# Kernel optimization log

Hardware: AMD Instinct MI355X
Metric: run time of the kernel (lower is better)

The kernel has to match this reference:

```python
import jax, jax.numpy as jnp
import numpy as np
from jax import lax

H = 666
W = 666
EPS = 1e-5


def _conv(x, w, b):
    # NCHW conv, SAME padding, stride 1
    y = lax.conv_general_dilated(x, w, (1, 1), 'SAME',
                                 dimension_numbers=('NCHW', 'OIHW', 'NCHW'))
    return y + b[None, :, None, None]


def _bn2d(x, g, b):
    m = jnp.mean(x, (0, 2, 3), keepdims=True)
    v = jnp.var(x, (0, 2, 3), keepdims=True)
    return (x - m) * lax.rsqrt(v + EPS) * g[None, :, None, None] + b[None, :, None, None]


def _pool(x):
    return lax.reduce_window(x, -jnp.inf, lax.max, (1, 1, 2, 2), (1, 1, 2, 2), 'VALID')


def setup_inputs() -> dict:
    key = jax.random.key(0)
    ks = jax.random.split(key, 16)
    P, N, D = 20000, 32, 9

    def rn(k, shape, scale=0.05):
        return (jax.random.normal(k, shape, jnp.float32) * scale).astype(jnp.float32)

    return {
        'pillars': jax.random.normal(ks[0], (P, N, D), jnp.float32),
        'coords': jax.random.randint(ks[1], (P, 3), 0, 666, jnp.int64 if jax.config.jax_enable_x64 else jnp.int32),
        # PillarFeatureNet
        'lin_w': rn(ks[2], (64, 9)), 'lin_b': jnp.zeros((64,), jnp.float32),
        'pfn_g': jnp.ones((64,), jnp.float32), 'pfn_b': jnp.zeros((64,), jnp.float32),
        # Backbone
        'c1_w': rn(ks[3], (64, 64, 3, 3)), 'c1_b': jnp.zeros((64,), jnp.float32),
        'bn1_g': jnp.ones((64,), jnp.float32), 'bn1_b': jnp.zeros((64,), jnp.float32),
        'c2_w': rn(ks[4], (128, 64, 3, 3)), 'c2_b': jnp.zeros((128,), jnp.float32),
        'bn2_g': jnp.ones((128,), jnp.float32), 'bn2_b': jnp.zeros((128,), jnp.float32),
        # SSD head
        'h1_w': rn(ks[5], (256, 128, 3, 3)), 'h1_b': jnp.zeros((256,), jnp.float32),
        'hbn_g': jnp.ones((256,), jnp.float32), 'hbn_b': jnp.zeros((256,), jnp.float32),
        'hb_w': rn(ks[6], (21, 256, 3, 3)), 'hb_b': jnp.zeros((21,), jnp.float32),
        'hc_w': rn(ks[7], (3, 256, 3, 3)), 'hc_b': jnp.zeros((3,), jnp.float32),
    }


def reference(pillars, coords, lin_w, lin_b, pfn_g, pfn_b,
              c1_w, c1_b, bn1_g, bn1_b, c2_w, c2_b, bn2_g, bn2_b,
              h1_w, h1_b, hbn_g, hbn_b, hb_w, hb_b, hc_w, hc_b):
    P, N, D = pillars.shape
    # --- PillarFeatureNet: Linear -> BN1d (batch stats) -> ReLU -> max over points ---
    x = pillars.reshape(P * N, D) @ lin_w.T + lin_b           # [P*N, 64]
    m = jnp.mean(x, 0)
    v = jnp.var(x, 0)
    x = jax.nn.relu((x - m) * lax.rsqrt(v + EPS) * pfn_g + pfn_b)
    feats = jnp.max(x.reshape(P, N, -1), axis=1)              # [P, 64]

    # --- PseudoImageScatter: one vectorized scatter replacing the per-pillar loop ---
    y_idx = coords[:, 1]
    x_idx = coords[:, 2]
    valid = (y_idx >= 0) & (y_idx < H) & (x_idx >= 0) & (x_idx < W)
    y_idx = jnp.where(valid, y_idx, H)   # OOB -> dropped by scatter
    x_idx = jnp.where(valid, x_idx, W)
    img = jnp.zeros((64, H, W), feats.dtype).at[:, y_idx, x_idx].set(feats.T, mode='drop')
    img = img[None]                                           # [1, 64, H, W]

    # --- Backbone ---
    b1 = _pool(jax.nn.relu(_bn2d(_conv(img, c1_w, c1_b), bn1_g, bn1_b)))   # [1,64,333,333]
    b2 = _pool(jax.nn.relu(_bn2d(_conv(b1, c2_w, c2_b), bn2_g, bn2_b)))    # [1,128,166,166]

    # --- SSD head ---
    h = jax.nn.relu(_bn2d(_conv(b2, h1_w, h1_b), hbn_g, hbn_b))            # [1,256,166,166]
    bbox = _conv(h, hb_w, hb_b)                                            # [1,21,166,166]
    cls = _conv(h, hc_w, hc_b)                                             # [1,3,166,166]
    return (bbox, cls)
```

## Files before the change

kernel.cpp:

```cpp
#include <hip/hip_runtime.h>
#include <hip/hip_bf16.h>
#include <cstdint>
#include <cstddef>

#define BN_EPS 1e-5f

typedef short short8 __attribute__((ext_vector_type(8)));
typedef float float16 __attribute__((ext_vector_type(16)));
typedef unsigned short ushort_t;

__device__ __forceinline__ float bf2f(ushort_t u) {
  return __uint_as_float(((unsigned int)u) << 16);
}
__device__ __forceinline__ ushort_t f2bf(float f) {
  unsigned int u = __float_as_uint(f);
  u += 0x7FFFu + ((u >> 16) & 1u);
  return (ushort_t)(u >> 16);
}


__global__ __launch_bounds__(512) void pillar_moments(
    const float* __restrict__ pillars, float* __restrict__ mom) {
  float S[9], M[45];
#pragma unroll
  for (int i = 0; i < 9; ++i) S[i] = 0.f;
#pragma unroll
  for (int i = 0; i < 45; ++i) M[i] = 0.f;
  const int t = blockIdx.x * 512 + threadIdx.x;
  const int NTH = 128 * 512;
  for (long r = t; r < 640000; r += NTH) {
    float x[9];
    const float* rp = pillars + r * 9;
#pragma unroll
    for (int d = 0; d < 9; ++d) x[d] = rp[d];
    int k = 0;
#pragma unroll
    for (int i = 0; i < 9; ++i) {
      S[i] += x[i];
#pragma unroll
      for (int j = i; j < 9; ++j) { M[k] += x[i] * x[j]; ++k; }
    }
  }
#pragma unroll
  for (int i = 0; i < 9; ++i)
#pragma unroll
    for (int o = 32; o > 0; o >>= 1) S[i] += __shfl_xor(S[i], o);
#pragma unroll
  for (int i = 0; i < 45; ++i)
#pragma unroll
    for (int o = 32; o > 0; o >>= 1) M[i] += __shfl_xor(M[i], o);
  __shared__ float red[8 * 54];
  int lane = threadIdx.x & 63, wv = threadIdx.x >> 6;
  if (lane == 0) {
#pragma unroll
    for (int i = 0; i < 9; ++i) red[wv * 54 + i] = S[i];
#pragma unroll
    for (int i = 0; i < 45; ++i) red[wv * 54 + 9 + i] = M[i];
  }
  __syncthreads();
  if (threadIdx.x < 54) {
    float s = 0.f;
#pragma unroll
    for (int w8 = 0; w8 < 8; ++w8) s += red[w8 * 54 + threadIdx.x];
    atomicAdd(&mom[threadIdx.x], s);
  }
}

__global__ void pfn_finalize(const float* __restrict__ mom,
                             const float* __restrict__ lin_w,
                             const float* __restrict__ lin_b,
                             const float* __restrict__ g, const float* __restrict__ b,
                             float* __restrict__ ss) {
  int c = threadIdx.x;
  double w[9], S[9];
#pragma unroll
  for (int d = 0; d < 9; ++d) {
    w[d] = (double)lin_w[c * 9 + d];
    S[d] = (double)mom[d];
  }
  double wS = 0.0;
#pragma unroll
  for (int d = 0; d < 9; ++d) wS += w[d] * S[d];
  double wMw = 0.0;
  int k = 0;
#pragma unroll
  for (int i = 0; i < 9; ++i)
#pragma unroll
    for (int j = i; j < 9; ++j) {
      double m = (double)mom[9 + k];
      wMw += (i == j ? 1.0 : 2.0) * w[i] * w[j] * m;
      ++k;
    }
  const double N = 640000.0;
  double bc = (double)lin_b[c];
  double mean = (wS + N * bc) / N;
  double ey2 = (wMw + 2.0 * bc * wS + N * bc * bc) / N;
  double var = ey2 - mean * mean;
  if (var < 0.0) var = 0.0;
  double inv = 1.0 / sqrt(var + (double)BN_EPS);
  double sc = (double)g[c] * inv;
  ss[c] = (float)sc;
  ss[c + 64] = (float)((double)b[c] - mean * sc);
}

__global__ __launch_bounds__(256) void pfn_feats(
    const float* __restrict__ pillars, const float* __restrict__ lin_w,
    const float* __restrict__ lin_b, const float* __restrict__ ss,
    ushort_t* __restrict__ feats) {
  __shared__ float s_p[1152];
  int tid = threadIdx.x;
  int c = tid & 63, pe = tid >> 6;
  long pb = (long)blockIdx.x * 4;
  for (int i = tid; i < 1152; i += 256) s_p[i] = pillars[pb * 288 + i];
  float w[9];
#pragma unroll
  for (int d = 0; d < 9; ++d) w[d] = lin_w[c * 9 + d];
  float bl = lin_b[c];
  float sc = ss[c], sh = ss[c + 64];
  __syncthreads();
  const float* pp = &s_p[pe * 288];
  float m = -1e30f;
#pragma unroll 4
  for (int n = 0; n < 32; ++n) {
    float y = bl;
#pragma unroll
    for (int d = 0; d < 9; ++d) y += pp[n * 9 + d] * w[d];
    float v = fmaxf(y * sc + sh, 0.f);
    m = fmaxf(m, v);
  }
  feats[(pb + pe) * 64 + c] = f2bf(m);
}


__global__ void scatter_winner(const int* __restrict__ coords, int* __restrict__ winner,
                               int P) {
  int p = blockIdx.x * 256 + threadIdx.x;
  if (p >= P) return;
  int y = coords[p * 3 + 1], x = coords[p * 3 + 2];
  if (y >= 0 && y < 666 && x >= 0 && x < 666) atomicMax(&winner[y * 666 + x], p);
}


__device__ __forceinline__ void prep_one(const float* __restrict__ w,
                                         ushort_t* __restrict__ w2, int C, int N,
                                         int Ntg, int chunks, int u) {
  int total = chunks * 9 * 2 * Ntg * 64;
  if (u >= total) return;
  int l = u & 63;
  int g = u >> 6;
  int ntg = g % Ntg;
  int g2 = g / Ntg;
  int s = g2 & 1;
  int g3 = g2 >> 1;
  int pos = g3 % 9;
  int cc = g3 / 9;
  int n = ntg * 32 + (l & 31);
  int c0 = cc * 32 + s * 16 + (l >> 5) * 8;
  ushort_t o8[8];
#pragma unroll
  for (int j = 0; j < 8; ++j) {
    int c = c0 + j;
    float v = (n < N && c < C) ? w[((size_t)n * C + c) * 9 + pos] : 0.f;
    o8[j] = f2bf(v);
  }
  *(uint4*)&w2[(size_t)u * 8] = *(const uint4*)o8;
}

__device__ __forceinline__ void prep_head_one(const float* __restrict__ hb,
                                              const float* __restrict__ hc,
                                              ushort_t* __restrict__ w2, int u) {
  int total = 8 * 9 * 2 * 64;
  if (u >= total) return;
  int l = u & 63;
  int g = u >> 6;
  int s = g & 1;
  int g3 = g >> 1;
  int pos = g3 % 9;
  int cc = g3 / 9;
  int n = l & 31;
  int c0 = cc * 32 + s * 16 + (l >> 5) * 8;
  ushort_t o8[8];
#pragma unroll
  for (int j = 0; j < 8; ++j) {
    int c = c0 + j;
    float v = 0.f;
    if (n < 21) v = hb[((size_t)n * 256 + c) * 9 + pos];
    else if (n < 24) v = hc[((size_t)(n - 21) * 256 + c) * 9 + pos];
    o8[j] = f2bf(v);
  }
  *(uint4*)&w2[(size_t)u * 8] = *(const uint4*)o8;
}

__global__ void prep_all(const float* __restrict__ c1_w, const float* __restrict__ c2_w,
                         const float* __restrict__ h1_w, const float* __restrict__ hb_w,
                         const float* __restrict__ hc_w, ushort_t* __restrict__ w2c1,
                         ushort_t* __restrict__ w2c2, ushort_t* __restrict__ w2h1,
                         ushort_t* __restrict__ w2hd) {
  int b = blockIdx.x;
  int t = threadIdx.x;
  if (b < 18) prep_one(c1_w, w2c1, 64, 64, 2, 2, b * 256 + t);
  else if (b < 54) prep_one(c2_w, w2c2, 64, 128, 4, 2, (b - 18) * 256 + t);
  else if (b < 198) prep_one(h1_w, w2h1, 128, 256, 8, 4, (b - 54) * 256 + t);
  else prep_head_one(hb_w, hc_w, w2hd, (b - 198) * 256 + t);
}


__global__ void bn_make_coefs(const float* __restrict__ acc, const float* __restrict__ g,
                              const float* __restrict__ b, float invN,
                              float* __restrict__ coef, int C) {
  int c = threadIdx.x;
  if (c >= C) return;
  float m = acc[c] * invN;
  float v = fmaxf(acc[c + 256] * invN - m * m, 0.f);
  float sc = g[c] * rsqrtf(v + BN_EPS);
  coef[c] = sc;
  coef[C + c] = b[c] - m * sc;
}


template <int NT, int WAVES, int MODE, bool HEAD, bool STATS, bool POOL>
__global__ __launch_bounds__(WAVES * 64, WAVES == 8 ? 4 : 3) void conv_mfma(
    const ushort_t* __restrict__ in, const int* __restrict__ winner,
    const ushort_t* __restrict__ feats, const ushort_t* __restrict__ w2,
    const float* __restrict__ bias, const float* __restrict__ bias2,
    const float* __restrict__ coef_in, ushort_t* __restrict__ obf,
    float* __restrict__ hpart, float* __restrict__ statacc, int W, int H, int C,
    int nchunks, int Ntg) {
  constexpr int NTHREADS = WAVES * 64;
  __shared__ ushort_t s_in[(WAVES + 2) * 66 * 32];
  __shared__ ushort_t s_w[9 * 2 * NT * 512];
  const int tid = threadIdx.x;
  const int lane = tid & 63, wv = tid >> 6;
  const int lc = lane & 31, lh = lane >> 5;
  const int x0 = blockIdx.x * 64, y0 = blockIdx.y * WAVES;
  const int z = blockIdx.z;
  const int cc0 = HEAD ? z * nchunks : 0;
  const int z_oc = HEAD ? 0 : z;

  int pc[2][2][3];
#pragma unroll
  for (int s = 0; s < 2; ++s)
#pragma unroll
    for (int Mt = 0; Mt < 2; ++Mt)
#pragma unroll
      for (int kx = 0; kx < 3; ++kx) {
        int col = Mt * 32 + kx + lc;
        int q = (2 * s + lh) ^ ((col >> 1) & 3);
        pc[s][Mt][kx] = col * 32 + q * 8;
      }

  const int sg = tid & 3;
  const int tpos = tid >> 2;
  constexpr int TPOS = NTHREADS / 4;
  constexpr int NPOS = (WAVES + 2) * 66;
  constexpr int NIT = (NPOS + TPOS - 1) / TPOS;
  int ldst[NIT], gsrc[NIT];
#pragma unroll
  for (int it = 0; it < NIT; ++it) {
    ldst[it] = -1;
    gsrc[it] = -1;
    int p = tpos + it * TPOS;
    if (p < NPOS) {
      int r = p / 66, col = p - r * 66;
      int f = sg ^ ((col >> 1) & 3);
      ldst[it] = (r * 66 + col) * 32 + f * 8;
      int gy = y0 - 1 + r, gx = x0 - 1 + col;
      if (gy >= 0 && gy < H && gx >= 0 && gx < W) {
        if (MODE == 2) {
          int pw = winner[gy * 666 + gx];
          if (pw >= 0) gsrc[it] = pw * 64 + sg * 8;
        } else {
          gsrc[it] = (gy * W + gx) * C + sg * 8;
        }
      }
    }
  }

  float bv[NT];
#pragma unroll
  for (int nt = 0; nt < NT; ++nt) {
    if (HEAD) {
      bv[nt] = (z == 0) ? (lc < 21 ? bias[lc] : (lc < 24 ? bias2[lc - 21] : 0.f)) : 0.f;
    } else {
      bv[nt] = bias[(z * NT + nt) * 32 + lc];
    }
  }
  float16 acc[2][NT];
#pragma unroll
  for (int Mt = 0; Mt < 2; ++Mt)
#pragma unroll
    for (int nt = 0; nt < NT; ++nt)
#pragma unroll
      for (int r = 0; r < 16; ++r) acc[Mt][nt][r] = bv[nt];

  for (int cc = 0; cc < nchunks; ++cc) {
    const int ccg = cc0 + cc;
    __syncthreads();
    if (MODE == 2) {
#pragma unroll
      for (int it = 0; it < NIT; ++it) {
        if (ldst[it] < 0) continue;
        uint4 v = make_uint4(0, 0, 0, 0);
        if (gsrc[it] >= 0) v = *(const uint4*)&feats[gsrc[it] + ccg * 32];
        *(uint4*)&s_in[ldst[it]] = v;
      }
    } else {
      float sc8[8], sh8[8];
      {
        int ch = ccg * 32 + sg * 8;
        float4 a0 = *(const float4*)&coef_in[ch];
        float4 a1 = *(const float4*)&coef_in[ch + 4];
        float4 b0 = *(const float4*)&coef_in[C + ch];
        float4 b1 = *(const float4*)&coef_in[C + ch + 4];
        sc8[0] = a0.x; sc8[1] = a0.y; sc8[2] = a0.z; sc8[3] = a0.w;
        sc8[4] = a1.x; sc8[5] = a1.y; sc8[6] = a1.z; sc8[7] = a1.w;
        sh8[0] = b0.x; sh8[1] = b0.y; sh8[2] = b0.z; sh8[3] = b0.w;
        sh8[4] = b1.x; sh8[5] = b1.y; sh8[6] = b1.z; sh8[7] = b1.w;
      }
#pragma unroll
      for (int it = 0; it < NIT; ++it) {
        if (ldst[it] < 0) continue;
        ushort_t v8[8] = {0, 0, 0, 0, 0, 0, 0, 0};
        if (gsrc[it] >= 0) {
          uint4 raw = *(const uint4*)&in[gsrc[it] + ccg * 32];
          const ushort_t* rp = (const ushort_t*)&raw;
#pragma unroll
          for (int j = 0; j < 8; ++j)
            v8[j] = f2bf(fmaxf(bf2f(rp[j]) * sc8[j] + sh8[j], 0.f));
        }
        *(uint4*)&s_in[ldst[it]] = *(const uint4*)v8;
      }
    }
    const int NW = NT * 1152;
    for (int u = tid; u < NW; u += NTHREADS) {
      int l16 = u & 63, grp = u >> 6;
      int nt = grp % NT, ps = grp / NT;
      const ushort_t* src =
          w2 + ((size_t)((ccg * 18 + ps) * Ntg + z_oc * NT + nt) * 64 + l16) * 8;
      *(uint4*)&s_w[(size_t)u * 8] = *(const uint4*)src;
    }
    __syncthreads();
#pragma unroll
    for (int ky = 0; ky < 3; ++ky) {
      int rowoff = (wv + ky) * (66 * 32);
#pragma unroll
      for (int kx = 0; kx < 3; ++kx) {
        const int pos = ky * 3 + kx;
#pragma unroll
        for (int s = 0; s < 2; ++s) {
          short8 Bf[NT];
#pragma unroll
          for (int nt = 0; nt < NT; ++nt)
            Bf[nt] = *(const short8*)&s_w[((pos * 2 + s) * NT + nt) * 512 + lane * 8];
#pragma unroll
          for (int Mt = 0; Mt < 2; ++Mt) {
            short8 Af = *(const short8*)&s_in[rowoff + pc[s][Mt][kx]];
#pragma unroll
            for (int nt = 0; nt < NT; ++nt)
              acc[Mt][nt] =
                  __builtin_amdgcn_mfma_f32_32x32x16_bf16(Af, Bf[nt], acc[Mt][nt], 0, 0, 0);
          }
        }
      }
    }
  }

  const int y = y0 + wv;
  const bool yok = (y < H);
  const int Ntot = Ntg * 32;

  if (HEAD) {
    if (yok) {
      float* hp = hpart + (size_t)z * (size_t)(H * W) * 32;
#pragma unroll
      for (int Mt = 0; Mt < 2; ++Mt)
#pragma unroll
        for (int r = 0; r < 16; ++r) {
          int m = (r & 3) + 8 * (r >> 2) + 4 * lh;
          int x = x0 + Mt * 32 + m;
          if (x < W) {
            size_t sp = (size_t)y * W + x;
            hp[sp * 32 + lc] = acc[Mt][0][r];
          }
        }
    }
    return;
  }

  if (!POOL) {
    if (yok) {
#pragma unroll
      for (int Mt = 0; Mt < 2; ++Mt)
#pragma unroll
        for (int r = 0; r < 16; ++r) {
          int m = (r & 3) + 8 * (r >> 2) + 4 * lh;
          int x = x0 + Mt * 32 + m;
          if (x < W) {
            size_t sp = (size_t)y * W + x;
#pragma unroll
            for (int nt = 0; nt < NT; ++nt) {
              int oc = (z * NT + nt) * 32 + lc;
              obf[sp * Ntot + oc] = f2bf(acc[Mt][nt][r]);
            }
          }
        }
    }
  }

  if (STATS) {
    float s1[NT], s2[NT];
#pragma unroll
    for (int nt = 0; nt < NT; ++nt) { s1[nt] = 0.f; s2[nt] = 0.f; }
    if (yok) {
#pragma unroll
      for (int Mt = 0; Mt < 2; ++Mt)
#pragma unroll
        for (int r = 0; r < 16; ++r) {
          int m = (r & 3) + 8 * (r >> 2) + 4 * lh;
          int x = x0 + Mt * 32 + m;
          if (x < W) {
#pragma unroll
            for (int nt = 0; nt < NT; ++nt) {
              float v = acc[Mt][nt][r];
              s1[nt] += v;
              s2[nt] += v * v;
            }
          }
        }
    }
#pragma unroll
    for (int nt = 0; nt < NT; ++nt) {
      s1[nt] += __shfl_xor(s1[nt], 32);
      s2[nt] += __shfl_xor(s2[nt], 32);
    }
    __syncthreads();
    float* red = (float*)s_in;
    if (lh == 0) {
#pragma unroll
      for (int nt = 0; nt < NT; ++nt) {
        red[(wv * NT + nt) * 32 + lc] = s1[nt];
        red[WAVES * NT * 32 + (wv * NT + nt) * 32 + lc] = s2[nt];
      }
    }
    __syncthreads();
    if (wv == 0 && lh == 0) {
#pragma unroll
      for (int nt = 0; nt < NT; ++nt) {
        float a = 0.f, b = 0.f;
#pragma unroll
        for (int w8 = 0; w8 < WAVES; ++w8) {
          a += red[(w8 * NT + nt) * 32 + lc];
          b += red[WAVES * NT * 32 + (w8 * NT + nt) * 32 + lc];
        }
        int ch = (z * NT + nt) * 32 + lc;
        atomicAdd(&statacc[ch], a);
        atomicAdd(&statacc[ch + 256], b);
      }
    }
  }

  if (POOL) {
    const int OWp = W >> 1, OHp = H >> 1;
    float hm[2][NT][8];
#pragma unroll
    for (int Mt = 0; Mt < 2; ++Mt)
#pragma unroll
      for (int nt = 0; nt < NT; ++nt)
#pragma unroll
        for (int i = 0; i < 8; ++i)
          hm[Mt][nt][i] = fmaxf(acc[Mt][nt][2 * i], acc[Mt][nt][2 * i + 1]);
    __syncthreads();
    float* pl = (float*)s_in;
    if (wv & 1) {
#pragma unroll
      for (int Mt = 0; Mt < 2; ++Mt)
#pragma unroll
        for (int nt = 0; nt < NT; ++nt)
#pragma unroll
          for (int i = 0; i < 8; ++i)
            pl[((((wv >> 1) * 2 + Mt) * NT + nt) * 8 + i) * 64 + lane] = hm[Mt][nt][i];
    }
    __syncthreads();
    if (!(wv & 1)) {
      int oy = (y0 + wv) >> 1;
      if (oy < OHp) {
#pragma unroll
        for (int Mt = 0; Mt < 2; ++Mt)
#pragma unroll
          for (int i = 0; i < 8; ++i) {
            int pxl = Mt * 16 + (i >> 1) * 4 + (i & 1) + 2 * lh;
            int ox = (x0 >> 1) + pxl;
            if (ox < OWp) {
#pragma unroll
              for (int nt = 0; nt < NT; ++nt) {
                float v = fmaxf(
                    hm[Mt][nt][i],
                    pl[((((wv >> 1) * 2 + Mt) * NT + nt) * 8 + i) * 64 + lane]);
                int oc = (z * NT + nt) * 32 + lc;
                obf[((size_t)oy * OWp + ox) * Ntot + oc] = f2bf(v);
              }
            }
          }
      }
    }
  }
}


__global__ __launch_bounds__(256) void head_reduce(const float* __restrict__ hp,
                                                   float* __restrict__ out, int HW,
                                                   int nz) {
  __shared__ float t[256 * 33];
  int tid = threadIdx.x;
  int sp0 = blockIdx.x * 256;
  int lim = (HW - sp0) * 32;
#pragma unroll 4
  for (int i = 0; i < 32; ++i) {
    int e = i * 256 + tid;
    float s = 0.f;
    if (e < lim) {
      size_t gidx = (size_t)sp0 * 32 + e;
      for (int z = 0; z < nz; ++z) s += hp[(size_t)z * HW * 32 + gidx];
    }
    t[(e >> 5) * 33 + (e & 31)] = s;
  }
  __syncthreads();
  int sp = sp0 + tid;
  if (sp < HW) {
#pragma unroll
    for (int ch = 0; ch < 24; ++ch)
      out[(size_t)ch * HW + sp] = t[tid * 33 + ch];
  }
}


extern "C" void kernel_launch(void* const* d_in, const int* in_sizes, int n_in,
                              void* d_out, int out_size, void* d_ws, size_t ws_size,
                              hipStream_t stream) {
  (void)in_sizes; (void)n_in; (void)out_size; (void)ws_size;
  const float* pillars = (const float*)d_in[0];
  const int* coords = (const int*)d_in[1];
  const float* lin_w = (const float*)d_in[2];
  const float* lin_b = (const float*)d_in[3];
  const float* pfn_g = (const float*)d_in[4];
  const float* pfn_b = (const float*)d_in[5];
  const float* c1_w = (const float*)d_in[6];
  const float* c1_b = (const float*)d_in[7];
  const float* bn1_g = (const float*)d_in[8];
  const float* bn1_b = (const float*)d_in[9];
  const float* c2_w = (const float*)d_in[10];
  const float* c2_b = (const float*)d_in[11];
  const float* bn2_g = (const float*)d_in[12];
  const float* bn2_b = (const float*)d_in[13];
  const float* h1_w = (const float*)d_in[14];
  const float* h1_b = (const float*)d_in[15];
  const float* hbn_g = (const float*)d_in[16];
  const float* hbn_b = (const float*)d_in[17];
  const float* hb_w = (const float*)d_in[18];
  const float* hb_b = (const float*)d_in[19];
  const float* hc_w = (const float*)d_in[20];
  const float* hc_b = (const float*)d_in[21];
  float* out = (float*)d_out;

  char* ws = (char*)d_ws;
  float* mom     = (float*)(ws + 0);
  float* pfn_ss  = (float*)(ws + 512);
  float* bn_acc1 = (float*)(ws + 1024);
  float* bn_acc2 = (float*)(ws + 3072);
  float* bn_acc3 = (float*)(ws + 5120);
  float* coef1   = (float*)(ws + 7168);
  float* coef2   = (float*)(ws + 7680);
  float* coef3   = (float*)(ws + 8704);
  int* winner    = (int*)(ws + 10752);
  ushort_t* feats  = (ushort_t*)(ws + 1785088);
  ushort_t* c1p    = (ushort_t*)(ws + 4345088);
  ushort_t* c2p    = (ushort_t*)(ws + 18538880);
  ushort_t* h1out  = (ushort_t*)(ws + 25593216);
  ushort_t* w2c1   = (ushort_t*)(ws + 39701888);
  ushort_t* w2c2   = (ushort_t*)(ws + 39775616);
  ushort_t* w2h1   = (ushort_t*)(ws + 39923072);
  ushort_t* w2hd   = (ushort_t*)(ws + 40512896);
  float* hpart     = (float*)(ws + 40660352);

  const int HW3 = 166 * 166;

  hipMemsetAsync(ws, 0, 10752, stream);
  hipMemsetAsync(winner, 0xFF, 1774224, stream);

  prep_all<<<234, 256, 0, stream>>>(c1_w, c2_w, h1_w, hb_w, hc_w, w2c1, w2c2, w2h1,
                                    w2hd);

  pillar_moments<<<128, 512, 0, stream>>>(pillars, mom);
  pfn_finalize<<<1, 64, 0, stream>>>(mom, lin_w, lin_b, pfn_g, pfn_b, pfn_ss);
  pfn_feats<<<5000, 256, 0, stream>>>(pillars, lin_w, lin_b, pfn_ss, feats);

  scatter_winner<<<(20000 + 255) / 256, 256, 0, stream>>>(coords, winner, 20000);

  conv_mfma<2, 8, 2, false, true, true><<<dim3(11, 84, 1), 512, 0, stream>>>(
      nullptr, winner, feats, w2c1, c1_b, nullptr, nullptr, c1p, nullptr, bn_acc1, 666,
      666, 64, 2, 2);
  bn_make_coefs<<<1, 64, 0, stream>>>(bn_acc1, bn1_g, bn1_b, 1.f / 443556.f, coef1, 64);

  conv_mfma<2, 8, 1, false, true, true><<<dim3(6, 42, 2), 512, 0, stream>>>(
      c1p, nullptr, nullptr, w2c2, c2_b, nullptr, coef1, c2p, nullptr, bn_acc2, 333, 333,
      64, 2, 4);
  bn_make_coefs<<<1, 128, 0, stream>>>(bn_acc2, bn2_g, bn2_b, 1.f / 110889.f, coef2, 128);

  conv_mfma<2, 4, 1, false, true, false><<<dim3(3, 42, 4), 256, 0, stream>>>(
      c2p, nullptr, nullptr, w2h1, h1_b, nullptr, coef2, h1out, nullptr, bn_acc3, 166,
      166, 128, 4, 8);
  bn_make_coefs<<<1, 256, 0, stream>>>(bn_acc3, hbn_g, hbn_b, 1.f / 27556.f, coef3, 256);

  conv_mfma<1, 4, 1, true, false, false><<<dim3(3, 42, 4), 256, 0, stream>>>(
      h1out, nullptr, nullptr, w2hd, hb_b, hc_b, coef3, nullptr, hpart, nullptr, 166,
      166, 256, 2, 1);
  head_reduce<<<(HW3 + 255) / 256, 256, 0, stream>>>(hpart, out, HW3, 4);
}
```

Before: 322.3 us.

## Split channel chunks into half-staging to shrink LDS and raise conv occupancy

```diff
diff --git a/kernel.cpp b/kernel.cpp
--- a/kernel.cpp
+++ b/kernel.cpp
@@ -218,8 +218,8 @@
 }
 
 
-template <int NT, int WAVES, int MODE, bool HEAD, bool STATS, bool POOL>
-__global__ __launch_bounds__(WAVES * 64, WAVES == 8 ? 4 : 3) void conv_mfma(
+template <int NT, int WAVES, int MODE, bool HEAD, bool STATS, bool POOL, bool SPLIT>
+__global__ __launch_bounds__(WAVES * 64, SPLIT ? 4 : (WAVES == 8 ? 4 : 3)) void conv_mfma(
     const ushort_t* __restrict__ in, const int* __restrict__ winner,
     const ushort_t* __restrict__ feats, const ushort_t* __restrict__ w2,
     const float* __restrict__ bias, const float* __restrict__ bias2,
@@ -227,8 +227,13 @@
     float* __restrict__ hpart, float* __restrict__ statacc, int W, int H, int C,
     int nchunks, int Ntg) {
   constexpr int NTHREADS = WAVES * 64;
-  __shared__ ushort_t s_in[(WAVES + 2) * 66 * 32];
-  __shared__ ushort_t s_w[9 * 2 * NT * 512];
+  constexpr int CPP = SPLIT ? 16 : 32;
+  constexpr int SGN = SPLIT ? 2 : 4;
+  constexpr int SIN = (WAVES + 2) * 66 * CPP;
+  constexpr int SWC = (SPLIT ? 9 : 18) * NT * 512;
+  __shared__ ushort_t s_all[SIN + SWC];
+  ushort_t* s_in = s_all;
+  ushort_t* s_w = s_all + SIN;
   const int tid = threadIdx.x;
   const int lane = tid & 63, wv = tid >> 6;
   const int lc = lane & 31, lh = lane >> 5;
@@ -245,13 +250,18 @@
 #pragma unroll
       for (int kx = 0; kx < 3; ++kx) {
         int col = Mt * 32 + kx + lc;
-        int q = (2 * s + lh) ^ ((col >> 1) & 3);
-        pc[s][Mt][kx] = col * 32 + q * 8;
-      }
-
-  const int sg = tid & 3;
-  const int tpos = tid >> 2;
-  constexpr int TPOS = NTHREADS / 4;
+        if (SPLIT) {
+          int q = lh ^ (col & 1);
+          pc[s][Mt][kx] = col * 16 + q * 8;
+        } else {
+          int q = (2 * s + lh) ^ ((col >> 1) & 3);
+          pc[s][Mt][kx] = col * 32 + q * 8;
+        }
+      }
+
+  const int sg = tid & (SGN - 1);
+  const int tpos = tid / SGN;
+  constexpr int TPOS = NTHREADS / SGN;
   constexpr int NPOS = (WAVES + 2) * 66;
   constexpr int NIT = (NPOS + TPOS - 1) / TPOS;
   int ldst[NIT], gsrc[NIT];
@@ -262,8 +272,8 @@
     int p = tpos + it * TPOS;
     if (p < NPOS) {
       int r = p / 66, col = p - r * 66;
-      int f = sg ^ ((col >> 1) & 3);
-      ldst[it] = (r * 66 + col) * 32 + f * 8;
+      int f = SPLIT ? (sg ^ (col & 1)) : (sg ^ ((col >> 1) & 3));
+      ldst[it] = (r * 66 + col) * CPP + f * 8;
       int gy = y0 - 1 + r, gx = x0 - 1 + col;
       if (gy >= 0 && gy < H && gx >= 0 && gx < W) {
         if (MODE == 2) {
@@ -293,21 +303,20 @@
 #pragma unroll
       for (int r = 0; r < 16; ++r) acc[Mt][nt][r] = bv[nt];
 
-  for (int cc = 0; cc < nchunks; ++cc) {
-    const int ccg = cc0 + cc;
-    __syncthreads();
+  auto stage_in = [&](int ccg, int sh) {
+    const int off = ccg * 32 + (SPLIT ? sh * 16 : 0);
     if (MODE == 2) {
 #pragma unroll
       for (int it = 0; it < NIT; ++it) {
         if (ldst[it] < 0) continue;
         uint4 v = make_uint4(0, 0, 0, 0);
-        if (gsrc[it] >= 0) v = *(const uint4*)&feats[gsrc[it] + ccg * 32];
+        if (gsrc[it] >= 0) v = *(const uint4*)&feats[gsrc[it] + off];
         *(uint4*)&s_in[ldst[it]] = v;
       }
     } else {
       float sc8[8], sh8[8];
       {
-        int ch = ccg * 32 + sg * 8;
+        int ch = off + sg * 8;
         float4 a0 = *(const float4*)&coef_in[ch];
         float4 a1 = *(const float4*)&coef_in[ch + 4];
         float4 b0 = *(const float4*)&coef_in[C + ch];
@@ -322,7 +331,7 @@
         if (ldst[it] < 0) continue;
         ushort_t v8[8] = {0, 0, 0, 0, 0, 0, 0, 0};
         if (gsrc[it] >= 0) {
-          uint4 raw = *(const uint4*)&in[gsrc[it] + ccg * 32];
+          uint4 raw = *(const uint4*)&in[gsrc[it] + off];
           const ushort_t* rp = (const ushort_t*)&raw;
 #pragma unroll
           for (int j = 0; j < 8; ++j)
@@ -331,18 +340,57 @@
         *(uint4*)&s_in[ldst[it]] = *(const uint4*)v8;
       }
     }
-    const int NW = NT * 1152;
-    for (int u = tid; u < NW; u += NTHREADS) {
-      int l16 = u & 63, grp = u >> 6;
-      int nt = grp % NT, ps = grp / NT;
-      const ushort_t* src =
-          w2 + ((size_t)((ccg * 18 + ps) * Ntg + z_oc * NT + nt) * 64 + l16) * 8;
-      *(uint4*)&s_w[(size_t)u * 8] = *(const uint4*)src;
-    }
-    __syncthreads();
+  };
+
+  auto stage_w = [&](int ccg, int sh) {
+    if (SPLIT) {
+      const int NWU = 9 * NT * 64;
+      for (int u = tid; u < NWU; u += NTHREADS) {
+        int l16 = u & 63, grp = u >> 6;
+        int nt = grp % NT, pos = grp / NT;
+        const ushort_t* src =
+            w2 + ((size_t)((ccg * 18 + pos * 2 + sh) * Ntg + z_oc * NT + nt) * 64 + l16) * 8;
+        *(uint4*)&s_w[(size_t)((pos * NT + nt) * 512 + l16 * 8)] = *(const uint4*)src;
+      }
+    } else {
+      const int NW = NT * 1152;
+      for (int u = tid; u < NW; u += NTHREADS) {
+        int l16 = u & 63, grp = u >> 6;
+        int nt = grp % NT, ps = grp / NT;
+        const ushort_t* src =
+            w2 + ((size_t)((ccg * 18 + ps) * Ntg + z_oc * NT + nt) * 64 + l16) * 8;
+        *(uint4*)&s_w[(size_t)u * 8] = *(const uint4*)src;
+      }
+    }
+  };
+
+  auto compute_half = [&]() {
 #pragma unroll
     for (int ky = 0; ky < 3; ++ky) {
-      int rowoff = (wv + ky) * (66 * 32);
+      int rowoff = (wv + ky) * (66 * CPP);
+#pragma unroll
+      for (int kx = 0; kx < 3; ++kx) {
+        const int pos = ky * 3 + kx;
+        short8 Bf[NT];
+#pragma unroll
+        for (int nt = 0; nt < NT; ++nt)
+          Bf[nt] = *(const short8*)&s_w[(pos * NT + nt) * 512 + lane * 8];
+#pragma unroll
+        for (int Mt = 0; Mt < 2; ++Mt) {
+          short8 Af = *(const short8*)&s_in[rowoff + pc[0][Mt][kx]];
+#pragma unroll
+          for (int nt = 0; nt < NT; ++nt)
+            acc[Mt][nt] =
+                __builtin_amdgcn_mfma_f32_32x32x16_bf16(Af, Bf[nt], acc[Mt][nt], 0, 0, 0);
+        }
+      }
+    }
+  };
+
+  auto compute_full = [&]() {
+#pragma unroll
+    for (int ky = 0; ky < 3; ++ky) {
+      int rowoff = (wv + ky) * (66 * CPP);
 #pragma unroll
       for (int kx = 0; kx < 3; ++kx) {
         const int pos = ky * 3 + kx;
@@ -362,6 +410,32 @@
           }
         }
       }
+    }
+  };
+
+  if (SPLIT) {
+    for (int cc = 0; cc < nchunks; ++cc) {
+#pragma unroll
+      for (int sh = 0; sh < 2; ++sh) {
+        __syncthreads();
+        stage_in(cc0 + cc, sh);
+        stage_w(cc0 + cc, sh);
+        __syncthreads();
+        __builtin_amdgcn_s_setprio(1);
+        compute_half();
+        __builtin_amdgcn_s_setprio(0);
+      }
+    }
+  } else {
+    for (int cc = 0; cc < nchunks; ++cc) {
+      const int ccg = cc0 + cc;
+      __syncthreads();
+      stage_in(ccg, 0);
+      stage_w(ccg, 0);
+      __syncthreads();
+      __builtin_amdgcn_s_setprio(1);
+      compute_full();
+      __builtin_amdgcn_s_setprio(0);
     }
   }
 
@@ -434,7 +508,7 @@
       s2[nt] += __shfl_xor(s2[nt], 32);
     }
     __syncthreads();
-    float* red = (float*)s_in;
+    float* red = (float*)s_all;
     if (lh == 0) {
 #pragma unroll
       for (int nt = 0; nt < NT; ++nt) {
@@ -470,7 +544,7 @@
         for (int i = 0; i < 8; ++i)
           hm[Mt][nt][i] = fmaxf(acc[Mt][nt][2 * i], acc[Mt][nt][2 * i + 1]);
     __syncthreads();
-    float* pl = (float*)s_in;
+    float* pl = (float*)s_all;
     if (wv & 1) {
 #pragma unroll
       for (int Mt = 0; Mt < 2; ++Mt)
@@ -596,22 +670,22 @@
 
   scatter_winner<<<(20000 + 255) / 256, 256, 0, stream>>>(coords, winner, 20000);
 
-  conv_mfma<2, 8, 2, false, true, true><<<dim3(11, 84, 1), 512, 0, stream>>>(
+  conv_mfma<2, 4, 2, false, true, true, true><<<dim3(11, 167, 1), 256, 0, stream>>>(
       nullptr, winner, feats, w2c1, c1_b, nullptr, nullptr, c1p, nullptr, bn_acc1, 666,
       666, 64, 2, 2);
   bn_make_coefs<<<1, 64, 0, stream>>>(bn_acc1, bn1_g, bn1_b, 1.f / 443556.f, coef1, 64);
 
-  conv_mfma<2, 8, 1, false, true, true><<<dim3(6, 42, 2), 512, 0, stream>>>(
+  conv_mfma<2, 4, 1, false, true, true, true><<<dim3(6, 84, 2), 256, 0, stream>>>(
       c1p, nullptr, nullptr, w2c2, c2_b, nullptr, coef1, c2p, nullptr, bn_acc2, 333, 333,
       64, 2, 4);
   bn_make_coefs<<<1, 128, 0, stream>>>(bn_acc2, bn2_g, bn2_b, 1.f / 110889.f, coef2, 128);
 
-  conv_mfma<2, 4, 1, false, true, false><<<dim3(3, 42, 4), 256, 0, stream>>>(
+  conv_mfma<2, 4, 1, false, true, false, false><<<dim3(3, 42, 4), 256, 0, stream>>>(
       c2p, nullptr, nullptr, w2h1, h1_b, nullptr, coef2, h1out, nullptr, bn_acc3, 166,
       166, 128, 4, 8);
   bn_make_coefs<<<1, 256, 0, stream>>>(bn_acc3, hbn_g, hbn_b, 1.f / 27556.f, coef3, 256);
 
-  conv_mfma<1, 4, 1, true, false, false><<<dim3(3, 42, 4), 256, 0, stream>>>(
+  conv_mfma<1, 4, 1, true, false, false, false><<<dim3(3, 42, 4), 256, 0, stream>>>(
       h1out, nullptr, nullptr, w2hd, hb_b, hc_b, coef3, nullptr, hpart, nullptr, 166,
       166, 256, 2, 1);
   head_reduce<<<(HW3 + 255) / 256, 256, 0, stream>>>(hpart, out, HW3, 4);
```

After: 350.6 us. 1.09x slower.

## Double-buffer conv staging with direct global-to-LDS loads and separate BN-ReLU pass

Applied to the files above, without the earlier changes.

```diff
diff --git a/kernel.cpp b/kernel.cpp
--- a/kernel.cpp
+++ b/kernel.cpp
@@ -16,6 +16,12 @@
   unsigned int u = __float_as_uint(f);
   u += 0x7FFFu + ((u >> 16) & 1u);
   return (ushort_t)(u >> 16);
+}
+
+__device__ __forceinline__ void gload16(const ushort_t* g, ushort_t* l) {
+  __builtin_amdgcn_global_load_lds(
+      (const __attribute__((address_space(1))) unsigned int*)g,
+      (__attribute__((address_space(3))) unsigned int*)l, 16, 0, 0);
 }
 
 
@@ -218,17 +224,45 @@
 }
 
 
-template <int NT, int WAVES, int MODE, bool HEAD, bool STATS, bool POOL>
-__global__ __launch_bounds__(WAVES * 64, WAVES == 8 ? 4 : 3) void conv_mfma(
+__global__ __launch_bounds__(256) void bnrelu(const ushort_t* __restrict__ inp,
+                                              const float* __restrict__ coef, int C,
+                                              int L8, ushort_t* __restrict__ outp) {
+  __shared__ float sc[512];
+  int tid = threadIdx.x;
+  for (int i = tid; i < 2 * C; i += 256) sc[i] = coef[i];
+  __syncthreads();
+  int t = blockIdx.x * 256 + tid;
+  if (t >= L8) return;
+  size_t e0 = (size_t)t * 8;
+  int c0 = (t << 3) & (C - 1);
+  short8 v = *(const short8*)&inp[e0];
+  const ushort_t* vp = (const ushort_t*)&v;
+  ushort_t o[8];
+#pragma unroll
+  for (int j = 0; j < 8; ++j) {
+    float x = bf2f(vp[j]);
+    o[j] = f2bf(fmaxf(x * sc[c0 + j] + sc[C + c0 + j], 0.f));
+  }
+  *(uint4*)&outp[e0] = *(const uint4*)o;
+}
+
+
+template <int NT, int WAVES, bool GATHER, bool HEAD, bool STATS, bool POOL>
+__global__ __launch_bounds__(WAVES * 64, 4) void conv_mfma(
     const ushort_t* __restrict__ in, const int* __restrict__ winner,
     const ushort_t* __restrict__ feats, const ushort_t* __restrict__ w2,
     const float* __restrict__ bias, const float* __restrict__ bias2,
-    const float* __restrict__ coef_in, ushort_t* __restrict__ obf,
+    const ushort_t* __restrict__ zbuf, ushort_t* __restrict__ obf,
     float* __restrict__ hpart, float* __restrict__ statacc, int W, int H, int C,
     int nchunks, int Ntg) {
   constexpr int NTHREADS = WAVES * 64;
-  __shared__ ushort_t s_in[(WAVES + 2) * 66 * 32];
-  __shared__ ushort_t s_w[9 * 2 * NT * 512];
+  constexpr int NPOS = (WAVES + 2) * 66;
+  constexpr int IN_U4 = NPOS * 2;
+  constexpr int W_U4 = 9 * NT * 64;
+  constexpr int INIT = (IN_U4 + NTHREADS - 1) / NTHREADS;
+  constexpr int WIT = (W_U4 + NTHREADS - 1) / NTHREADS;
+  __shared__ ushort_t s_in[2][IN_U4 * 8];
+  __shared__ ushort_t s_w[2][W_U4 * 8];
   const int tid = threadIdx.x;
   const int lane = tid & 63, wv = tid >> 6;
   const int lc = lane & 31, lh = lane >> 5;
@@ -237,42 +271,44 @@
   const int cc0 = HEAD ? z * nchunks : 0;
   const int z_oc = HEAD ? 0 : z;
 
-  int pc[2][2][3];
-#pragma unroll
-  for (int s = 0; s < 2; ++s)
-#pragma unroll
-    for (int Mt = 0; Mt < 2; ++Mt)
-#pragma unroll
-      for (int kx = 0; kx < 3; ++kx) {
-        int col = Mt * 32 + kx + lc;
-        int q = (2 * s + lh) ^ ((col >> 1) & 3);
-        pc[s][Mt][kx] = col * 32 + q * 8;
-      }
-
-  const int sg = tid & 3;
-  const int tpos = tid >> 2;
-  constexpr int TPOS = NTHREADS / 4;
-  constexpr int NPOS = (WAVES + 2) * 66;
-  constexpr int NIT = (NPOS + TPOS - 1) / TPOS;
-  int ldst[NIT], gsrc[NIT];
-#pragma unroll
-  for (int it = 0; it < NIT; ++it) {
-    ldst[it] = -1;
-    gsrc[it] = -1;
-    int p = tpos + it * TPOS;
-    if (p < NPOS) {
+  int pc[2][3];
+#pragma unroll
+  for (int Mt = 0; Mt < 2; ++Mt)
+#pragma unroll
+    for (int kx = 0; kx < 3; ++kx) {
+      int col = Mt * 32 + kx + lc;
+      pc[Mt][kx] = col * 16 + (lh ^ (col & 1)) * 8;
+    }
+
+  const ushort_t* isrc[INIT];
+#pragma unroll
+  for (int it = 0; it < INIT; ++it) {
+    isrc[it] = zbuf;
+    int d = it * NTHREADS + tid;
+    if (d < IN_U4) {
+      int p = d >> 1, g = d & 1;
       int r = p / 66, col = p - r * 66;
-      int f = sg ^ ((col >> 1) & 3);
-      ldst[it] = (r * 66 + col) * 32 + f * 8;
+      int cg = g ^ (col & 1);
       int gy = y0 - 1 + r, gx = x0 - 1 + col;
       if (gy >= 0 && gy < H && gx >= 0 && gx < W) {
-        if (MODE == 2) {
+        if (GATHER) {
           int pw = winner[gy * 666 + gx];
-          if (pw >= 0) gsrc[it] = pw * 64 + sg * 8;
+          if (pw >= 0) isrc[it] = feats + pw * 64 + cg * 8;
         } else {
-          gsrc[it] = (gy * W + gx) * C + sg * 8;
+          isrc[it] = in + (size_t)(gy * W + gx) * C + cg * 8;
         }
       }
+    }
+  }
+  int wof[WIT];
+#pragma unroll
+  for (int it = 0; it < WIT; ++it) {
+    wof[it] = 0;
+    int d = it * NTHREADS + tid;
+    if (d < W_U4) {
+      int grp = d >> 6, l16 = d & 63;
+      int pos = grp / NT, nt = grp % NT;
+      wof[it] = (pos * 2 * Ntg + z_oc * NT + nt) * 512 + l16 * 8;
     }
   }
 
@@ -293,76 +329,55 @@
 #pragma unroll
       for (int r = 0; r < 16; ++r) acc[Mt][nt][r] = bv[nt];
 
-  for (int cc = 0; cc < nchunks; ++cc) {
-    const int ccg = cc0 + cc;
-    __syncthreads();
-    if (MODE == 2) {
-#pragma unroll
-      for (int it = 0; it < NIT; ++it) {
-        if (ldst[it] < 0) continue;
-        uint4 v = make_uint4(0, 0, 0, 0);
-        if (gsrc[it] >= 0) v = *(const uint4*)&feats[gsrc[it] + ccg * 32];
-        *(uint4*)&s_in[ldst[it]] = v;
-      }
-    } else {
-      float sc8[8], sh8[8];
-      {
-        int ch = ccg * 32 + sg * 8;
-        float4 a0 = *(const float4*)&coef_in[ch];
-        float4 a1 = *(const float4*)&coef_in[ch + 4];
-        float4 b0 = *(const float4*)&coef_in[C + ch];
-        float4 b1 = *(const float4*)&coef_in[C + ch + 4];
-        sc8[0] = a0.x; sc8[1] = a0.y; sc8[2] = a0.z; sc8[3] = a0.w;
-        sc8[4] = a1.x; sc8[5] = a1.y; sc8[6] = a1.z; sc8[7] = a1.w;
-        sh8[0] = b0.x; sh8[1] = b0.y; sh8[2] = b0.z; sh8[3] = b0.w;
-        sh8[4] = b1.x; sh8[5] = b1.y; sh8[6] = b1.z; sh8[7] = b1.w;
-      }
-#pragma unroll
-      for (int it = 0; it < NIT; ++it) {
-        if (ldst[it] < 0) continue;
-        ushort_t v8[8] = {0, 0, 0, 0, 0, 0, 0, 0};
-        if (gsrc[it] >= 0) {
-          uint4 raw = *(const uint4*)&in[gsrc[it] + ccg * 32];
-          const ushort_t* rp = (const ushort_t*)&raw;
-#pragma unroll
-          for (int j = 0; j < 8; ++j)
-            v8[j] = f2bf(fmaxf(bf2f(rp[j]) * sc8[j] + sh8[j], 0.f));
-        }
-        *(uint4*)&s_in[ldst[it]] = *(const uint4*)v8;
-      }
-    }
-    const int NW = NT * 1152;
-    for (int u = tid; u < NW; u += NTHREADS) {
-      int l16 = u & 63, grp = u >> 6;
-      int nt = grp % NT, ps = grp / NT;
-      const ushort_t* src =
-          w2 + ((size_t)((ccg * 18 + ps) * Ntg + z_oc * NT + nt) * 64 + l16) * 8;
-      *(uint4*)&s_w[(size_t)u * 8] = *(const uint4*)src;
-    }
-    __syncthreads();
+  auto stage = [&](int ph, int b) {
+    int ccg = cc0 + (ph >> 1), sh = ph & 1;
+    int coff = ccg * 32 + sh * 16;
+#pragma unroll
+    for (int it = 0; it < INIT; ++it) {
+      int d = it * NTHREADS + tid;
+      if (d < IN_U4)
+        gload16(isrc[it] + coff, &s_in[b][(size_t)(it * NTHREADS + wv * 64) * 8]);
+    }
+    int wbase = (ccg * 18 + sh) * Ntg * 512;
+#pragma unroll
+    for (int it = 0; it < WIT; ++it) {
+      int d = it * NTHREADS + tid;
+      if (d < W_U4)
+        gload16(w2 + wbase + wof[it], &s_w[b][(size_t)(it * NTHREADS + wv * 64) * 8]);
+    }
+  };
+
+  auto compute_phase = [&](int b) {
 #pragma unroll
     for (int ky = 0; ky < 3; ++ky) {
-      int rowoff = (wv + ky) * (66 * 32);
+      const ushort_t* rowp = &s_in[b][(wv + ky) * (66 * 16)];
 #pragma unroll
       for (int kx = 0; kx < 3; ++kx) {
         const int pos = ky * 3 + kx;
-#pragma unroll
-        for (int s = 0; s < 2; ++s) {
-          short8 Bf[NT];
+        short8 Bf[NT];
+#pragma unroll
+        for (int nt = 0; nt < NT; ++nt)
+          Bf[nt] = *(const short8*)&s_w[b][(pos * NT + nt) * 512 + lane * 8];
+#pragma unroll
+        for (int Mt = 0; Mt < 2; ++Mt) {
+          short8 Af = *(const short8*)&rowp[pc[Mt][kx]];
 #pragma unroll
           for (int nt = 0; nt < NT; ++nt)
-            Bf[nt] = *(const short8*)&s_w[((pos * 2 + s) * NT + nt) * 512 + lane * 8];
-#pragma unroll
-          for (int Mt = 0; Mt < 2; ++Mt) {
-            short8 Af = *(const short8*)&s_in[rowoff + pc[s][Mt][kx]];
-#pragma unroll
-            for (int nt = 0; nt < NT; ++nt)
-              acc[Mt][nt] =
-                  __builtin_amdgcn_mfma_f32_32x32x16_bf16(Af, Bf[nt], acc[Mt][nt], 0, 0, 0);
-          }
+            acc[Mt][nt] =
+                __builtin_amdgcn_mfma_f32_32x32x16_bf16(Af, Bf[nt], acc[Mt][nt], 0, 0, 0);
         }
       }
     }
+  };
+
+  const int nph = nchunks * 2;
+  stage(0, 0);
+  for (int ph = 0; ph < nph; ++ph) {
+    asm volatile("s_waitcnt vmcnt(0)\n\ts_barrier" ::: "memory");
+    if (ph + 1 < nph) stage(ph + 1, (ph + 1) & 1);
+    __builtin_amdgcn_s_setprio(1);
+    compute_phase(ph & 1);
+    __builtin_amdgcn_s_setprio(0);
   }
 
   const int y = y0 + wv;
@@ -571,20 +586,24 @@
   float* coef1   = (float*)(ws + 7168);
   float* coef2   = (float*)(ws + 7680);
   float* coef3   = (float*)(ws + 8704);
-  int* winner    = (int*)(ws + 10752);
-  ushort_t* feats  = (ushort_t*)(ws + 1785088);
-  ushort_t* c1p    = (ushort_t*)(ws + 4345088);
-  ushort_t* c2p    = (ushort_t*)(ws + 18538880);
-  ushort_t* h1out  = (ushort_t*)(ws + 25593216);
-  ushort_t* w2c1   = (ushort_t*)(ws + 39701888);
-  ushort_t* w2c2   = (ushort_t*)(ws + 39775616);
-  ushort_t* w2h1   = (ushort_t*)(ws + 39923072);
-  ushort_t* w2hd   = (ushort_t*)(ws + 40512896);
-  float* hpart     = (float*)(ws + 40660352);
+  ushort_t* zbuf = (ushort_t*)(ws + 10752);
+  int* winner    = (int*)(ws + 11264);
+  ushort_t* feats  = (ushort_t*)(ws + 1785600);
+  ushort_t* c1p    = (ushort_t*)(ws + 4345600);
+  ushort_t* c2a    = (ushort_t*)(ws + 4345600);
+  ushort_t* c2p    = (ushort_t*)(ws + 18539392);
+  ushort_t* h1out  = (ushort_t*)(ws + 25593728);
+  ushort_t* w2c1   = (ushort_t*)(ws + 39702400);
+  ushort_t* w2c2   = (ushort_t*)(ws + 39776128);
+  ushort_t* w2h1   = (ushort_t*)(ws + 39923584);
+  ushort_t* w2hd   = (ushort_t*)(ws + 40513408);
+  float* hpart     = (float*)(ws + 40660864);
+  ushort_t* c1a    = (ushort_t*)(ws + 54769536);
+  ushort_t* h1a    = (ushort_t*)(ws + 54769536);
 
   const int HW3 = 166 * 166;
 
-  hipMemsetAsync(ws, 0, 10752, stream);
+  hipMemsetAsync(ws, 0, 11264, stream);
   hipMemsetAsync(winner, 0xFF, 1774224, stream);
 
   prep_all<<<234, 256, 0, stream>>>(c1_w, c2_w, h1_w, hb_w, hc_w, w2c1, w2c2, w2h1,
@@ -596,23 +615,29 @@
 
   scatter_winner<<<(20000 + 255) / 256, 256, 0, stream>>>(coords, winner, 20000);
 
-  conv_mfma<2, 8, 2, false, true, true><<<dim3(11, 84, 1), 512, 0, stream>>>(
-      nullptr, winner, feats, w2c1, c1_b, nullptr, nullptr, c1p, nullptr, bn_acc1, 666,
+  conv_mfma<2, 8, true, false, true, true><<<dim3(11, 84, 1), 512, 0, stream>>>(
+      nullptr, winner, feats, w2c1, c1_b, nullptr, zbuf, c1p, nullptr, bn_acc1, 666,
       666, 64, 2, 2);
   bn_make_coefs<<<1, 64, 0, stream>>>(bn_acc1, bn1_g, bn1_b, 1.f / 443556.f, coef1, 64);
 
-  conv_mfma<2, 8, 1, false, true, true><<<dim3(6, 42, 2), 512, 0, stream>>>(
-      c1p, nullptr, nullptr, w2c2, c2_b, nullptr, coef1, c2p, nullptr, bn_acc2, 333, 333,
+  bnrelu<<<(887112 + 255) / 256, 256, 0, stream>>>(c1p, coef1, 64, 887112, c1a);
+
+  conv_mfma<2, 8, false, false, true, true><<<dim3(6, 42, 2), 512, 0, stream>>>(
+      c1a, nullptr, nullptr, w2c2, c2_b, nullptr, zbuf, c2p, nullptr, bn_acc2, 333, 333,
       64, 2, 4);
   bn_make_coefs<<<1, 128, 0, stream>>>(bn_acc2, bn2_g, bn2_b, 1.f / 110889.f, coef2, 128);
 
-  conv_mfma<2, 4, 1, false, true, false><<<dim3(3, 42, 4), 256, 0, stream>>>(
-      c2p, nullptr, nullptr, w2h1, h1_b, nullptr, coef2, h1out, nullptr, bn_acc3, 166,
+  bnrelu<<<(440896 + 255) / 256, 256, 0, stream>>>(c2p, coef2, 128, 440896, c2a);
+
+  conv_mfma<2, 4, false, false, true, false><<<dim3(3, 42, 4), 256, 0, stream>>>(
+      c2a, nullptr, nullptr, w2h1, h1_b, nullptr, zbuf, h1out, nullptr, bn_acc3, 166,
       166, 128, 4, 8);
   bn_make_coefs<<<1, 256, 0, stream>>>(bn_acc3, hbn_g, hbn_b, 1.f / 27556.f, coef3, 256);
 
-  conv_mfma<1, 4, 1, true, false, false><<<dim3(3, 42, 4), 256, 0, stream>>>(
-      h1out, nullptr, nullptr, w2hd, hb_b, hc_b, coef3, nullptr, hpart, nullptr, 166,
+  bnrelu<<<(881792 + 255) / 256, 256, 0, stream>>>(h1out, coef3, 256, 881792, h1a);
+
+  conv_mfma<1, 4, false, true, false, false><<<dim3(3, 42, 4), 256, 0, stream>>>(
+      h1a, nullptr, nullptr, w2hd, hb_b, hc_b, zbuf, nullptr, hpart, nullptr, 166,
       166, 256, 2, 1);
   head_reduce<<<(HW3 + 255) / 256, 256, 0, stream>>>(hpart, out, HW3, 4);
 }
```

After: 323.0 us. Within noise of the previous version (+0.2%).
